# Kernel tuning notes

Hardware: AMD Instinct MI355X
Metric: run time of the kernel (lower is better)

Reference implementation:

```python
import jax, jax.numpy as jnp
import numpy as np
import math

B, S, D, H = 1, 512, 2048, 16
HD = D // H
E, I, G, TKG, TK = 64, 512, 8, 4, 6
SH_I = 2 * I  # n_shared_experts * moe_inter_dim
ROUTE_SCALE = 2.5
EPS = 1e-5
THETA = 500000.0


def rms_norm(x, w):
    return x * jax.lax.rsqrt(jnp.mean(x * x, axis=-1, keepdims=True) + EPS) * w


def rope(x, cos, sin):
    # x: [B,S,H,HD]; complex pairing matches torch.view_as_complex on reshape(..., HD//2, 2)
    xr = x.reshape(x.shape[:-1] + (HD // 2, 2))
    re, im = xr[..., 0], xr[..., 1]
    c = cos[None, :, None, :]
    s = sin[None, :, None, :]
    out = jnp.stack([re * c - im * s, re * s + im * c], axis=-1)
    return out.reshape(x.shape)


def forward(x, freqs_cos, freqs_sin, mask, attn_norm_w, ffn_norm_w,
            wq, wk, wv, wo, gate_w, exp_w1, exp_w2, exp_w3,
            sh_w1, sh_w2, sh_w3):
    # ---- attention sub-block ----
    h = rms_norm(x, attn_norm_w)
    q = (h @ wq.T).reshape(B, S, H, HD)
    k = (h @ wk.T).reshape(B, S, H, HD)
    v = (h @ wv.T).reshape(B, S, H, HD)
    q = rope(q, freqs_cos, freqs_sin)
    k = rope(k, freqs_cos, freqs_sin)
    scores = jnp.einsum('bqhd,bkhd->bhqk', q, k) / math.sqrt(HD) + mask
    p = jax.nn.softmax(scores.astype(jnp.float32), axis=-1).astype(q.dtype)
    attn = jnp.einsum('bhqk,bkhd->bqhd', p, v).reshape(B, S, D)
    x1 = x + attn @ wo.T

    # ---- MoE sub-block ----
    t = rms_norm(x1, ffn_norm_w).reshape(-1, D)  # [T,D]
    T = t.shape[0]
    s = jax.nn.sigmoid(t @ gate_w.T)             # [T,E] sigmoid scoring, bias=None
    sg = s.reshape(T, G, E // G)
    group_scores = sg.max(axis=-1)               # amax per group (bias is None)
    _, gidx = jax.lax.top_k(group_scores, TKG)   # top-4 groups
    keep = jax.nn.one_hot(gidx, G, dtype=s.dtype).sum(axis=1) > 0  # [T,G]
    masked = jnp.where(keep[:, :, None], sg, -jnp.inf).reshape(T, E)
    _, idx = jax.lax.top_k(masked, TK)           # top-6 experts within kept groups
    w = jnp.take_along_axis(s, idx, axis=1)      # gather original scores
    w = w / w.sum(axis=-1, keepdims=True) * ROUTE_SCALE

    # dense combine weights (scatter of top-k routing weights)
    gate_dense = jnp.zeros((T, E), x.dtype).at[jnp.arange(T)[:, None], idx].add(w)

    # routed experts: SwiGLU per expert, weighted combine
    h1 = jnp.einsum('td,eid->tei', t, exp_w1)    # [T,E,I]
    h3 = jnp.einsum('td,eid->tei', t, exp_w3)
    a = jax.nn.silu(h1) * h3
    routed = jnp.einsum('tei,edi,te->td', a, exp_w2, gate_dense)

    # shared experts MLP
    shared = (jax.nn.silu(t @ sh_w1.T) * (t @ sh_w3.T)) @ sh_w2.T

    return x1 + (routed + shared).reshape(B, S, D)


def setup_inputs() -> dict:
    key = jax.random.key(0)
    ks = jax.random.split(key, 12)
    sc = 0.02
    x = jax.random.normal(ks[0], (B, S, D), jnp.float32)
    inv = 1.0 / (THETA ** (jnp.arange(0, HD, 2, dtype=jnp.float32) / HD))
    ang = jnp.arange(S, dtype=jnp.float32)[:, None] * inv[None, :]
    freqs_cos = jnp.cos(ang)
    freqs_sin = jnp.sin(ang)
    mask = jnp.triu(jnp.full((S, S), -1e9, jnp.float32), k=1)[None, None]
    return {
        'x': x,
        'freqs_cos': freqs_cos,
        'freqs_sin': freqs_sin,
        'mask': mask,
        'attn_norm_w': jnp.ones((D,), jnp.float32),
        'ffn_norm_w': jnp.ones((D,), jnp.float32),
        'wq': jax.random.normal(ks[1], (D, D), jnp.float32) * sc,
        'wk': jax.random.normal(ks[2], (D, D), jnp.float32) * sc,
        'wv': jax.random.normal(ks[3], (D, D), jnp.float32) * sc,
        'wo': jax.random.normal(ks[4], (D, D), jnp.float32) * sc,
        'gate_w': jax.random.normal(ks[5], (E, D), jnp.float32) * sc,
        'exp_w1': jax.random.normal(ks[6], (E, I, D), jnp.float32) * sc,
        'exp_w2': jax.random.normal(ks[7], (E, D, I), jnp.float32) * sc,
        'exp_w3': jax.random.normal(ks[8], (E, I, D), jnp.float32) * sc,
        'sh_w1': jax.random.normal(ks[9], (SH_I, D), jnp.float32) * sc,
        'sh_w2': jax.random.normal(ks[10], (D, SH_I), jnp.float32) * sc,
        'sh_w3': jax.random.normal(ks[11], (SH_I, D), jnp.float32) * sc,
    }


def reference(x, freqs_cos, freqs_sin, mask, attn_norm_w, ffn_norm_w,
              wq, wk, wv, wo, gate_w, exp_w1, exp_w2, exp_w3,
              sh_w1, sh_w2, sh_w3):
    return forward(x, freqs_cos, freqs_sin, mask, attn_norm_w, ffn_norm_w,
                   wq, wk, wv, wo, gate_w, exp_w1, exp_w2, exp_w3,
                   sh_w1, sh_w2, sh_w3)
```

## Files before the change

### kernel.cpp

```cpp
#include <hip/hip_runtime.h>
#include <hip/hip_bf16.h>
#include <math.h>

constexpr int S   = 512;
constexpr int D   = 2048;
constexpr int H   = 16;
constexpr int HD  = 128;
constexpr int T   = 512;
constexpr int E   = 64;
constexpr int I_  = 512;
constexpr int G   = 8;
constexpr int TKG = 4;
constexpr int TK  = 6;
constexpr int SH_I = 1024;
constexpr float ROUTE_SCALE = 2.5f;
constexpr float EPS = 1e-5f;

typedef short   s16x8   __attribute__((ext_vector_type(8)));
typedef unsigned short ushort8 __attribute__((ext_vector_type(8)));
typedef float   f32x4   __attribute__((ext_vector_type(4)));

__device__ inline void split8(const float4& x0, const float4& x1, ushort8& h, ushort8& l) {
    float xs[8] = {x0.x, x0.y, x0.z, x0.w, x1.x, x1.y, x1.z, x1.w};
#pragma unroll
    for (int j = 0; j < 8; ++j) {
        __bf16 hb = (__bf16)xs[j];
        float hf = (float)hb;
        __bf16 lb = (__bf16)(xs[j] - hf);
        h[j] = __builtin_bit_cast(unsigned short, hb);
        l[j] = __builtin_bit_cast(unsigned short, lb);
    }
}

__device__ inline s16x8 ldsfrag(const unsigned short* p) {
    return *(const s16x8*)p;
}

__global__ __launch_bounds__(256) void rmsnorm_kernel(const float* __restrict__ x,
                                                      const float* __restrict__ w,
                                                      float* __restrict__ out) {
    int t = blockIdx.x;
    int tid = threadIdx.x;
    const float* row = x + (size_t)t * D;
    float ss = 0.f;
    for (int i = tid; i < D; i += 256) { float v = row[i]; ss += v * v; }
    for (int o = 32; o; o >>= 1) ss += __shfl_down(ss, o, 64);
    __shared__ float red[4];
    if ((tid & 63) == 0) red[tid >> 6] = ss;
    __syncthreads();
    float tot = red[0] + red[1] + red[2] + red[3];
    float scale = rsqrtf(tot / (float)D + EPS);
    for (int i = tid; i < D; i += 256) out[(size_t)t * D + i] = row[i] * scale * w[i];
}

__global__ __launch_bounds__(256) void mgemm_nt_kernel(const float* __restrict__ A,
                                                       const float* __restrict__ B0,
                                                       const float* __restrict__ B1,
                                                       const float* __restrict__ B2,
                                                       float* __restrict__ C0,
                                                       float* __restrict__ C1,
                                                       float* __restrict__ C2,
                                                       const float* __restrict__ addsrc,
                                                       int M, int N, int K) {
    (void)M;
    const float* B = (blockIdx.z == 0) ? B0 : ((blockIdx.z == 1) ? B1 : B2);
    float*       C = (blockIdx.z == 0) ? C0 : ((blockIdx.z == 1) ? C1 : C2);
    __shared__ unsigned short Ah[64][40], Al[64][40], Bh[64][40], Bl[64][40];
    const int m0 = blockIdx.y * 64, n0 = blockIdx.x * 64;
    const int tid = threadIdx.x;
    const int w = tid >> 6, lane = tid & 63;
    const int srow = tid >> 2;
    const int skq  = (tid & 3) * 8;
    const int wm = (w >> 1) * 32, wn = (w & 1) * 32;
    const int fr = lane >> 4, fc = lane & 15;
    const float* Arow = A + (size_t)(m0 + srow) * K + skq;
    const float* Brow = B + (size_t)(n0 + srow) * K + skq;

    f32x4 acc[2][2] = {};
    const int KT = K >> 5;
    float4 pa0 = *(const float4*)(Arow);
    float4 pa1 = *(const float4*)(Arow + 4);
    float4 pb0 = *(const float4*)(Brow);
    float4 pb1 = *(const float4*)(Brow + 4);

    for (int kt = 0; kt < KT; ++kt) {
        __syncthreads();
        {
            ushort8 h, l;
            split8(pa0, pa1, h, l);
            *(ushort8*)&Ah[srow][skq] = h; *(ushort8*)&Al[srow][skq] = l;
            split8(pb0, pb1, h, l);
            *(ushort8*)&Bh[srow][skq] = h; *(ushort8*)&Bl[srow][skq] = l;
        }
        __syncthreads();
        if (kt + 1 < KT) {
            const float* An = Arow + (kt + 1) * 32;
            const float* Bn = Brow + (kt + 1) * 32;
            pa0 = *(const float4*)(An); pa1 = *(const float4*)(An + 4);
            pb0 = *(const float4*)(Bn); pb1 = *(const float4*)(Bn + 4);
        }
        s16x8 fah[2], fal[2], fbh[2], fbl[2];
#pragma unroll
        for (int mf = 0; mf < 2; ++mf) {
            int r = wm + mf * 16 + fc;
            fah[mf] = ldsfrag(&Ah[r][fr * 8]);
            fal[mf] = ldsfrag(&Al[r][fr * 8]);
        }
#pragma unroll
        for (int nf = 0; nf < 2; ++nf) {
            int r = wn + nf * 16 + fc;
            fbh[nf] = ldsfrag(&Bh[r][fr * 8]);
            fbl[nf] = ldsfrag(&Bl[r][fr * 8]);
        }
#pragma unroll
        for (int mf = 0; mf < 2; ++mf)
#pragma unroll
            for (int nf = 0; nf < 2; ++nf) {
                acc[mf][nf] = __builtin_amdgcn_mfma_f32_16x16x32_bf16(fah[mf], fbh[nf], acc[mf][nf], 0, 0, 0);
                acc[mf][nf] = __builtin_amdgcn_mfma_f32_16x16x32_bf16(fah[mf], fbl[nf], acc[mf][nf], 0, 0, 0);
                acc[mf][nf] = __builtin_amdgcn_mfma_f32_16x16x32_bf16(fal[mf], fbh[nf], acc[mf][nf], 0, 0, 0);
            }
    }

#pragma unroll
    for (int mf = 0; mf < 2; ++mf)
#pragma unroll
        for (int nf = 0; nf < 2; ++nf)
#pragma unroll
            for (int r = 0; r < 4; ++r) {
                int gm = m0 + wm + mf * 16 + fr * 4 + r;
                int gn = n0 + wn + nf * 16 + fc;
                size_t off = (size_t)gm * N + gn;
                float v = acc[mf][nf][r];
                if (addsrc) v += addsrc[off];
                C[off] = v;
            }
}

__global__ __launch_bounds__(256) void rope_kernel(float* __restrict__ q, float* __restrict__ k,
                                                   const float* __restrict__ fc,
                                                   const float* __restrict__ fs) {
    int idx = blockIdx.x * 256 + threadIdx.x;
    int p  = idx & (HD / 2 - 1);
    int hh = (idx >> 6) & (H - 1);
    int t  = idx >> 10;
    float c = fc[t * (HD / 2) + p], s = fs[t * (HD / 2) + p];
    size_t base = (size_t)t * D + hh * HD + p * 2;
    float re = q[base], im = q[base + 1];
    q[base]     = re * c - im * s;
    q[base + 1] = re * s + im * c;
    re = k[base]; im = k[base + 1];
    k[base]     = re * c - im * s;
    k[base + 1] = re * s + im * c;
}

__global__ __launch_bounds__(256) void attn_kernel(const float* __restrict__ q,
                                                   const float* __restrict__ k,
                                                   const float* __restrict__ v,
                                                   float* __restrict__ o) {
    int qi = blockIdx.x, hh = blockIdx.y, tid = threadIdx.x;
    __shared__ float qs[HD];
    __shared__ float sc[S];
    __shared__ float redm[4];
    __shared__ float redz[4];
    __shared__ float part[256];
    if (tid < HD) qs[tid] = q[(size_t)qi * D + hh * HD + tid];
    __syncthreads();
    int kn = qi + 1;
    float lmax = -1e30f;
    for (int kk = tid; kk < kn; kk += 256) {
        const float4* k4 = (const float4*)(k + (size_t)kk * D + hh * HD);
        const float4* q4 = (const float4*)qs;
        float s = 0.f;
#pragma unroll
        for (int d4 = 0; d4 < HD / 4; d4++) {
            float4 kvv = k4[d4], qvv = q4[d4];
            s += qvv.x * kvv.x + qvv.y * kvv.y + qvv.z * kvv.z + qvv.w * kvv.w;
        }
        s *= 0.08838834764831845f;
        sc[kk] = s;
        lmax = fmaxf(lmax, s);
    }
    for (int o2 = 32; o2; o2 >>= 1) lmax = fmaxf(lmax, __shfl_down(lmax, o2, 64));
    if ((tid & 63) == 0) redm[tid >> 6] = lmax;
    __syncthreads();
    float M_ = fmaxf(fmaxf(redm[0], redm[1]), fmaxf(redm[2], redm[3]));
    float lsum = 0.f;
    for (int kk = tid; kk < kn; kk += 256) {
        float e2 = expf(sc[kk] - M_);
        sc[kk] = e2;
        lsum += e2;
    }
    for (int o2 = 32; o2; o2 >>= 1) lsum += __shfl_down(lsum, o2, 64);
    if ((tid & 63) == 0) redz[tid >> 6] = lsum;
    __syncthreads();
    float Z = redz[0] + redz[1] + redz[2] + redz[3];
    int d2 = tid & (HD - 1);
    int halfsel = tid >> 7;
    float acc = 0.f;
    for (int kk = halfsel; kk < kn; kk += 2)
        acc += sc[kk] * v[(size_t)kk * D + hh * HD + d2];
    part[tid] = acc;
    __syncthreads();
    if (tid < HD) o[(size_t)qi * D + hh * HD + tid] = (part[tid] + part[tid + HD]) / Z;
}

__global__ __launch_bounds__(256) void gate_kernel(const float* __restrict__ tbuf,
                                                   const float* __restrict__ gate_w,
                                                   float* __restrict__ logits) {
    int tok = blockIdx.x;
    int e    = threadIdx.x >> 2;
    int part = threadIdx.x & 3;
    const float* trow = tbuf   + (size_t)tok * D;
    const float* wrow = gate_w + (size_t)e * D;
    float s = 0.f;
    for (int k = part * 4; k < D; k += 16) {
        float4 a = *(const float4*)(trow + k);
        float4 b = *(const float4*)(wrow + k);
        s += a.x * b.x + a.y * b.y + a.z * b.z + a.w * b.w;
    }
    s += __shfl_down(s, 1, 4);
    s += __shfl_down(s, 2, 4);
    if (part == 0) logits[(size_t)tok * E + e] = s;
}

__global__ __launch_bounds__(64) void routing_kernel(const float* __restrict__ logits,
                                                     float* __restrict__ gw,
                                                     int* __restrict__ counts,
                                                     int* __restrict__ elist) {
    int t = blockIdx.x;
    int lane = threadIdx.x;
    __shared__ float ss[E];
    if (lane < E) ss[lane] = 1.f / (1.f + expf(-logits[(size_t)t * E + lane]));
    __syncthreads();
    if (lane == 0) {
        float gs[G];
        for (int g = 0; g < G; g++) {
            float m = ss[g * 8];
            for (int j = 1; j < 8; j++) m = fmaxf(m, ss[g * 8 + j]);
            gs[g] = m;
        }
        bool keep[G];
        for (int g = 0; g < G; g++) keep[g] = false;
        for (int r = 0; r < TKG; r++) {
            int best = -1; float bv = -1e30f;
            for (int g = 0; g < G; g++)
                if (!keep[g] && gs[g] > bv) { bv = gs[g]; best = g; }
            keep[best] = true;
        }
        float masked[E];
        for (int e2 = 0; e2 < E; e2++) masked[e2] = keep[e2 >> 3] ? ss[e2] : -1e30f;
        int chosen[TK]; float w[TK]; float wsum = 0.f;
        for (int r = 0; r < TK; r++) {
            int best = 0; float bv = -1e31f;
            for (int e2 = 0; e2 < E; e2++)
                if (masked[e2] > bv) { bv = masked[e2]; best = e2; }
            chosen[r] = best; w[r] = ss[best]; masked[best] = -1e31f; wsum += w[r];
        }
        float scale_ = ROUTE_SCALE / wsum;
        for (int r = 0; r < TK; r++) {
            int slot = t * TK + r;
            gw[slot] = w[r] * scale_;
            int e2 = chosen[r];
            int pos = atomicAdd(&counts[e2], 1);
            elist[e2 * T + pos] = slot;
        }
    }
}

__global__ __launch_bounds__(256) void moe_up_kernel(const float* __restrict__ tbuf,
                                                     const float* __restrict__ w1,
                                                     const float* __restrict__ w3,
                                                     const int* __restrict__ counts,
                                                     const int* __restrict__ elist,
                                                     float* __restrict__ abuf) {
    const int e = blockIdx.x;
    const int nt = counts[e];
    if (nt == 0) return;
    const int i0 = blockIdx.y * 64;
    const float* W1 = w1 + (size_t)e * I_ * D;
    const float* W3 = w3 + (size_t)e * I_ * D;
    __shared__ unsigned short Ah[64][40], Al[64][40];
    __shared__ unsigned short B1h[64][40], B1l[64][40];
    __shared__ unsigned short B3h[64][40], B3l[64][40];
    __shared__ int slots[64];
    __shared__ const float* rows[64];
    const int tid = threadIdx.x;
    const int w = tid >> 6, lane = tid & 63;
    const int srow = tid >> 2;
    const int skq  = (tid & 3) * 8;
    const int wm = (w >> 1) * 32, wn = (w & 1) * 32;
    const int fr = lane >> 4, fc = lane & 15;
    const float* B1row = W1 + (size_t)(i0 + srow) * D + skq;
    const float* B3row = W3 + (size_t)(i0 + srow) * D + skq;
    const float4 z4 = make_float4(0.f, 0.f, 0.f, 0.f);
    const int KT = D >> 5;

    for (int tb = 0; tb < nt; tb += 64) {
        if (tid < 64) {
            int sl = (tb + tid < nt) ? elist[e * T + tb + tid] : -1;
            slots[tid] = sl;
            rows[tid] = (sl >= 0) ? (tbuf + (size_t)(sl / TK) * D) : nullptr;
        }
        __syncthreads();
        const float* Ap = rows[srow];
        f32x4 c1[2][2] = {}, c3[2][2] = {};
        float4 pa0, pa1, p10, p11, p30, p31;
        pa0 = Ap ? *(const float4*)(Ap + skq)     : z4;
        pa1 = Ap ? *(const float4*)(Ap + skq + 4) : z4;
        p10 = *(const float4*)(B1row);
        p11 = *(const float4*)(B1row + 4);
        p30 = *(const float4*)(B3row);
        p31 = *(const float4*)(B3row + 4);

        for (int kt = 0; kt < KT; ++kt) {
            __syncthreads();
            {
                ushort8 h, l;
                split8(pa0, pa1, h, l);
                *(ushort8*)&Ah[srow][skq] = h; *(ushort8*)&Al[srow][skq] = l;
                split8(p10, p11, h, l);
                *(ushort8*)&B1h[srow][skq] = h; *(ushort8*)&B1l[srow][skq] = l;
                split8(p30, p31, h, l);
                *(ushort8*)&B3h[srow][skq] = h; *(ushort8*)&B3l[srow][skq] = l;
            }
            __syncthreads();
            if (kt + 1 < KT) {
                const int ko = (kt + 1) * 32 + skq;
                pa0 = Ap ? *(const float4*)(Ap + ko)     : z4;
                pa1 = Ap ? *(const float4*)(Ap + ko + 4) : z4;
                p10 = *(const float4*)(B1row + (kt + 1) * 32);
                p11 = *(const float4*)(B1row + (kt + 1) * 32 + 4);
                p30 = *(const float4*)(B3row + (kt + 1) * 32);
                p31 = *(const float4*)(B3row + (kt + 1) * 32 + 4);
            }
            s16x8 fah[2], fal[2], f1h[2], f1l[2], f3h[2], f3l[2];
#pragma unroll
            for (int mf = 0; mf < 2; ++mf) {
                int r = wm + mf * 16 + fc;
                fah[mf] = ldsfrag(&Ah[r][fr * 8]);
                fal[mf] = ldsfrag(&Al[r][fr * 8]);
            }
#pragma unroll
            for (int nf = 0; nf < 2; ++nf) {
                int r = wn + nf * 16 + fc;
                f1h[nf] = ldsfrag(&B1h[r][fr * 8]);
                f1l[nf] = ldsfrag(&B1l[r][fr * 8]);
                f3h[nf] = ldsfrag(&B3h[r][fr * 8]);
                f3l[nf] = ldsfrag(&B3l[r][fr * 8]);
            }
#pragma unroll
            for (int mf = 0; mf < 2; ++mf)
#pragma unroll
                for (int nf = 0; nf < 2; ++nf) {
                    c1[mf][nf] = __builtin_amdgcn_mfma_f32_16x16x32_bf16(fah[mf], f1h[nf], c1[mf][nf], 0, 0, 0);
                    c1[mf][nf] = __builtin_amdgcn_mfma_f32_16x16x32_bf16(fah[mf], f1l[nf], c1[mf][nf], 0, 0, 0);
                    c1[mf][nf] = __builtin_amdgcn_mfma_f32_16x16x32_bf16(fal[mf], f1h[nf], c1[mf][nf], 0, 0, 0);
                    c3[mf][nf] = __builtin_amdgcn_mfma_f32_16x16x32_bf16(fah[mf], f3h[nf], c3[mf][nf], 0, 0, 0);
                    c3[mf][nf] = __builtin_amdgcn_mfma_f32_16x16x32_bf16(fah[mf], f3l[nf], c3[mf][nf], 0, 0, 0);
                    c3[mf][nf] = __builtin_amdgcn_mfma_f32_16x16x32_bf16(fal[mf], f3h[nf], c3[mf][nf], 0, 0, 0);
                }
        }

#pragma unroll
        for (int mf = 0; mf < 2; ++mf)
#pragma unroll
            for (int nf = 0; nf < 2; ++nf)
#pragma unroll
                for (int r = 0; r < 4; ++r) {
                    int mrow = wm + mf * 16 + fr * 4 + r;
                    if (tb + mrow < nt) {
                        int sl = slots[mrow];
                        float h1 = c1[mf][nf][r];
                        float h3 = c3[mf][nf][r];
                        float o = (h1 / (1.f + expf(-h1))) * h3;
                        abuf[(size_t)sl * I_ + i0 + wn + nf * 16 + fc] = o;
                    }
                }
        __syncthreads();
    }
}

__global__ __launch_bounds__(256) void moe_down_kernel(const float* __restrict__ abuf,
                                                       const float* __restrict__ w2,
                                                       const int* __restrict__ counts,
                                                       const int* __restrict__ elist,
                                                       const float* __restrict__ gw,
                                                       float* __restrict__ routed) {
    const int e = blockIdx.x;
    const int nt = counts[e];
    if (nt == 0) return;
    const int d0 = blockIdx.y * 64;
    const float* W2 = w2 + (size_t)e * D * I_;
    __shared__ unsigned short Ah[64][40], Al[64][40], Bh[64][40], Bl[64][40];
    __shared__ int slots[64];
    __shared__ const float* rows[64];
    const int tid = threadIdx.x;
    const int w = tid >> 6, lane = tid & 63;
    const int srow = tid >> 2;
    const int skq  = (tid & 3) * 8;
    const int wm = (w >> 1) * 32, wn = (w & 1) * 32;
    const int fr = lane >> 4, fc = lane & 15;
    const float* Brow = W2 + (size_t)(d0 + srow) * I_ + skq;
    const float4 z4 = make_float4(0.f, 0.f, 0.f, 0.f);
    const int KT = I_ >> 5;

    for (int tb = 0; tb < nt; tb += 64) {
        if (tid < 64) {
            int sl = (tb + tid < nt) ? elist[e * T + tb + tid] : -1;
            slots[tid] = sl;
            rows[tid] = (sl >= 0) ? (abuf + (size_t)sl * I_) : nullptr;
        }
        __syncthreads();
        const float* Ap = rows[srow];
        f32x4 acc[2][2] = {};
        float4 pa0, pa1, pb0, pb1;
        pa0 = Ap ? *(const float4*)(Ap + skq)     : z4;
        pa1 = Ap ? *(const float4*)(Ap + skq + 4) : z4;
        pb0 = *(const float4*)(Brow);
        pb1 = *(const float4*)(Brow + 4);

        for (int kt = 0; kt < KT; ++kt) {
            __syncthreads();
            {
                ushort8 h, l;
                split8(pa0, pa1, h, l);
                *(ushort8*)&Ah[srow][skq] = h; *(ushort8*)&Al[srow][skq] = l;
                split8(pb0, pb1, h, l);
                *(ushort8*)&Bh[srow][skq] = h; *(ushort8*)&Bl[srow][skq] = l;
            }
            __syncthreads();
            if (kt + 1 < KT) {
                const int ko = (kt + 1) * 32 + skq;
                pa0 = Ap ? *(const float4*)(Ap + ko)     : z4;
                pa1 = Ap ? *(const float4*)(Ap + ko + 4) : z4;
                pb0 = *(const float4*)(Brow + (kt + 1) * 32);
                pb1 = *(const float4*)(Brow + (kt + 1) * 32 + 4);
            }
            s16x8 fah[2], fal[2], fbh[2], fbl[2];
#pragma unroll
            for (int mf = 0; mf < 2; ++mf) {
                int r = wm + mf * 16 + fc;
                fah[mf] = ldsfrag(&Ah[r][fr * 8]);
                fal[mf] = ldsfrag(&Al[r][fr * 8]);
            }
#pragma unroll
            for (int nf = 0; nf < 2; ++nf) {
                int r = wn + nf * 16 + fc;
                fbh[nf] = ldsfrag(&Bh[r][fr * 8]);
                fbl[nf] = ldsfrag(&Bl[r][fr * 8]);
            }
#pragma unroll
            for (int mf = 0; mf < 2; ++mf)
#pragma unroll
                for (int nf = 0; nf < 2; ++nf) {
                    acc[mf][nf] = __builtin_amdgcn_mfma_f32_16x16x32_bf16(fah[mf], fbh[nf], acc[mf][nf], 0, 0, 0);
                    acc[mf][nf] = __builtin_amdgcn_mfma_f32_16x16x32_bf16(fah[mf], fbl[nf], acc[mf][nf], 0, 0, 0);
                    acc[mf][nf] = __builtin_amdgcn_mfma_f32_16x16x32_bf16(fal[mf], fbh[nf], acc[mf][nf], 0, 0, 0);
                }
        }

#pragma unroll
        for (int mf = 0; mf < 2; ++mf)
#pragma unroll
            for (int nf = 0; nf < 2; ++nf)
#pragma unroll
                for (int r = 0; r < 4; ++r) {
                    int mrow = wm + mf * 16 + fr * 4 + r;
                    if (tb + mrow < nt) {
                        int sl = slots[mrow];
                        float g = gw[sl];
                        int t = sl / TK;
                        atomicAdd(&routed[(size_t)t * D + d0 + wn + nf * 16 + fc], g * acc[mf][nf][r]);
                    }
                }
        __syncthreads();
    }
}

__global__ __launch_bounds__(256) void silu_mul_kernel(const float* __restrict__ a,
                                                       const float* __restrict__ b,
                                                       float* __restrict__ o, int n) {
    int i = blockIdx.x * 256 + threadIdx.x;
    if (i < n) { float x = a[i]; o[i] = x / (1.f + expf(-x)) * b[i]; }
}

__global__ __launch_bounds__(256) void add_inplace_kernel(float* __restrict__ o,
                                                          const float* __restrict__ a, int n) {
    int i = blockIdx.x * 256 + threadIdx.x;
    if (i < n) o[i] += a[i];
}

extern "C" void kernel_launch(void* const* d_in, const int* in_sizes, int n_in,
                              void* d_out, int out_size, void* d_ws, size_t ws_size,
                              hipStream_t stream) {
    (void)in_sizes; (void)n_in; (void)out_size; (void)ws_size;
    const float* x      = (const float*)d_in[0];
    const float* fc     = (const float*)d_in[1];
    const float* fs     = (const float*)d_in[2];
    const float* anw    = (const float*)d_in[4];
    const float* fnw    = (const float*)d_in[5];
    const float* wq     = (const float*)d_in[6];
    const float* wk     = (const float*)d_in[7];
    const float* wv     = (const float*)d_in[8];
    const float* wo     = (const float*)d_in[9];
    const float* gate_w = (const float*)d_in[10];
    const float* ew1    = (const float*)d_in[11];
    const float* ew2    = (const float*)d_in[12];
    const float* ew3    = (const float*)d_in[13];
    const float* sw1    = (const float*)d_in[14];
    const float* sw2    = (const float*)d_in[15];
    const float* sw3    = (const float*)d_in[16];
    float* out = (float*)d_out;

    char* wsp = (char*)d_ws;
    size_t off = 0;
    auto alloc = [&](size_t bytes) {
        void* p = wsp + off;
        off += (bytes + 255) & ~(size_t)255;
        return p;
    };
    float* hbuf   = (float*)alloc((size_t)T * D * 4);
    float* qbuf   = (float*)alloc((size_t)T * D * 4);
    float* kbuf   = (float*)alloc((size_t)T * D * 4);
    float* vbuf   = (float*)alloc((size_t)T * D * 4);
    float* attnb  = (float*)alloc((size_t)T * D * 4);
    float* x1     = (float*)alloc((size_t)T * D * 4);
    float* tbuf   = (float*)alloc((size_t)T * D * 4);
    float* routed = (float*)alloc((size_t)T * D * 4);
    float* logits = (float*)alloc((size_t)T * E * 4);
    float* gwbuf  = (float*)alloc((size_t)T * TK * 4);
    int*   counts = (int*)alloc(E * 4);
    int*   elist  = (int*)alloc((size_t)E * T * 4);
    float* abuf   = (float*)alloc((size_t)T * TK * I_ * 4);
    float* u1     = (float*)alloc((size_t)T * SH_I * 4);
    float* u3     = (float*)alloc((size_t)T * SH_I * 4);
    float* ub     = (float*)alloc((size_t)T * SH_I * 4);

    hipMemsetAsync(counts, 0, E * 4, stream);
    hipMemsetAsync(routed, 0, (size_t)T * D * 4, stream);

    rmsnorm_kernel<<<T, 256, 0, stream>>>(x, anw, hbuf);
    mgemm_nt_kernel<<<dim3(D / 64, T / 64, 3), 256, 0, stream>>>(hbuf, wq, wk, wv,
                                                                 qbuf, kbuf, vbuf,
                                                                 nullptr, T, D, D);
    rope_kernel<<<(T * H * HD / 2) / 256, 256, 0, stream>>>(qbuf, kbuf, fc, fs);
    attn_kernel<<<dim3(S, H), 256, 0, stream>>>(qbuf, kbuf, vbuf, attnb);
    mgemm_nt_kernel<<<dim3(D / 64, T / 64, 1), 256, 0, stream>>>(attnb, wo, wo, wo,
                                                                 x1, x1, x1,
                                                                 x, T, D, D);

    rmsnorm_kernel<<<T, 256, 0, stream>>>(x1, fnw, tbuf);
    gate_kernel<<<T, 256, 0, stream>>>(tbuf, gate_w, logits);
    routing_kernel<<<T, 64, 0, stream>>>(logits, gwbuf, counts, elist);
    moe_up_kernel<<<dim3(E, I_ / 64), 256, 0, stream>>>(tbuf, ew1, ew3, counts, elist, abuf);
    moe_down_kernel<<<dim3(E, D / 64), 256, 0, stream>>>(abuf, ew2, counts, elist, gwbuf, routed);

    mgemm_nt_kernel<<<dim3(SH_I / 64, T / 64, 2), 256, 0, stream>>>(tbuf, sw1, sw3, sw3,
                                                                    u1, u3, u3,
                                                                    nullptr, T, SH_I, D);
    silu_mul_kernel<<<(T * SH_I) / 256, 256, 0, stream>>>(u1, u3, ub, T * SH_I);
    mgemm_nt_kernel<<<dim3(D / 64, T / 64, 1), 256, 0, stream>>>(ub, sw2, sw2, sw2,
                                                                 out, out, out,
                                                                 x1, T, D, SH_I);
    add_inplace_kernel<<<(T * D) / 256, 256, 0, stream>>>(out, routed, T * D);
}
```

Before: 1.678 ms.

## Replace scalar attention with tiled flash-attention using split-bf16 MFMA

```diff
diff --git a/kernel.cpp b/kernel.cpp
--- a/kernel.cpp
+++ b/kernel.cpp
@@ -34,6 +34,10 @@
 
 __device__ inline s16x8 ldsfrag(const unsigned short* p) {
     return *(const s16x8*)p;
+}
+
+__device__ inline s16x8 as_s16(ushort8 u) {
+    return __builtin_bit_cast(s16x8, u);
 }
 
 __global__ __launch_bounds__(256) void rmsnorm_kernel(const float* __restrict__ x,
@@ -154,55 +158,133 @@
     k[base + 1] = re * s + im * c;
 }
 
-__global__ __launch_bounds__(256) void attn_kernel(const float* __restrict__ q,
-                                                   const float* __restrict__ k,
-                                                   const float* __restrict__ v,
-                                                   float* __restrict__ o) {
-    int qi = blockIdx.x, hh = blockIdx.y, tid = threadIdx.x;
-    __shared__ float qs[HD];
-    __shared__ float sc[S];
-    __shared__ float redm[4];
-    __shared__ float redz[4];
-    __shared__ float part[256];
-    if (tid < HD) qs[tid] = q[(size_t)qi * D + hh * HD + tid];
-    __syncthreads();
-    int kn = qi + 1;
-    float lmax = -1e30f;
-    for (int kk = tid; kk < kn; kk += 256) {
-        const float4* k4 = (const float4*)(k + (size_t)kk * D + hh * HD);
-        const float4* q4 = (const float4*)qs;
-        float s = 0.f;
-#pragma unroll
-        for (int d4 = 0; d4 < HD / 4; d4++) {
-            float4 kvv = k4[d4], qvv = q4[d4];
-            s += qvv.x * kvv.x + qvv.y * kvv.y + qvv.z * kvv.z + qvv.w * kvv.w;
-        }
-        s *= 0.08838834764831845f;
-        sc[kk] = s;
-        lmax = fmaxf(lmax, s);
-    }
-    for (int o2 = 32; o2; o2 >>= 1) lmax = fmaxf(lmax, __shfl_down(lmax, o2, 64));
-    if ((tid & 63) == 0) redm[tid >> 6] = lmax;
-    __syncthreads();
-    float M_ = fmaxf(fmaxf(redm[0], redm[1]), fmaxf(redm[2], redm[3]));
-    float lsum = 0.f;
-    for (int kk = tid; kk < kn; kk += 256) {
-        float e2 = expf(sc[kk] - M_);
-        sc[kk] = e2;
-        lsum += e2;
-    }
-    for (int o2 = 32; o2; o2 >>= 1) lsum += __shfl_down(lsum, o2, 64);
-    if ((tid & 63) == 0) redz[tid >> 6] = lsum;
-    __syncthreads();
-    float Z = redz[0] + redz[1] + redz[2] + redz[3];
-    int d2 = tid & (HD - 1);
-    int halfsel = tid >> 7;
-    float acc = 0.f;
-    for (int kk = halfsel; kk < kn; kk += 2)
-        acc += sc[kk] * v[(size_t)kk * D + hh * HD + d2];
-    part[tid] = acc;
-    __syncthreads();
-    if (tid < HD) o[(size_t)qi * D + hh * HD + tid] = (part[tid] + part[tid + HD]) / Z;
+__global__ __launch_bounds__(256) void attn_mfma_kernel(const float* __restrict__ q,
+                                                        const float* __restrict__ k,
+                                                        const float* __restrict__ v,
+                                                        float* __restrict__ o) {
+    const int qt = blockIdx.x, h = blockIdx.y;
+    const int q0 = qt * 64;
+    const int tid = threadIdx.x;
+    const int w = tid >> 6, lane = tid & 63;
+    const int fc = lane & 15, fr = lane >> 4;
+    __shared__ unsigned short Kh[4][32][40], Kl[4][32][40];
+    __shared__ unsigned short Vth[128][44], Vtl[128][44];
+    __shared__ unsigned short Pbh[4][16][38], Pbl[4][16][38];
+
+    ushort8 qh[4], ql[4];
+    {
+        const float* qrow = q + (size_t)(q0 + w * 16 + fc) * D + h * HD;
+#pragma unroll
+        for (int ks = 0; ks < 4; ++ks) {
+            float4 a = *(const float4*)(qrow + ks * 32 + fr * 8);
+            float4 b = *(const float4*)(qrow + ks * 32 + fr * 8 + 4);
+            split8(a, b, qh[ks], ql[ks]);
+        }
+    }
+
+    f32x4 accO[8] = {};
+    float mold[4] = {-3e38f, -3e38f, -3e38f, -3e38f};
+    float lsum[4] = {};
+    const int NT = 2 * qt + 2;
+
+    for (int kt = 0; kt < NT; ++kt) {
+        const int k0 = kt * 32;
+        __syncthreads();
+#pragma unroll
+        for (int rep = 0; rep < 2; ++rep) {
+            int e = rep * 256 + tid;
+            int key = e >> 4;
+            int dq  = (e & 15) * 8;
+            const float* kr = k + (size_t)(k0 + key) * D + h * HD + dq;
+            const float* vr = v + (size_t)(k0 + key) * D + h * HD + dq;
+            float4 a = *(const float4*)kr, b = *(const float4*)(kr + 4);
+            ushort8 hh, ll;
+            split8(a, b, hh, ll);
+            *(ushort8*)&Kh[dq >> 5][key][dq & 31] = hh;
+            *(ushort8*)&Kl[dq >> 5][key][dq & 31] = ll;
+            a = *(const float4*)vr; b = *(const float4*)(vr + 4);
+            split8(a, b, hh, ll);
+#pragma unroll
+            for (int j = 0; j < 8; ++j) { Vth[dq + j][key] = hh[j]; Vtl[dq + j][key] = ll[j]; }
+        }
+        __syncthreads();
+
+        f32x4 sc[2] = {};
+#pragma unroll
+        for (int kf = 0; kf < 2; ++kf) {
+#pragma unroll
+            for (int ks = 0; ks < 4; ++ks) {
+                s16x8 kbh = ldsfrag(&Kh[ks][kf * 16 + fc][fr * 8]);
+                s16x8 kbl = ldsfrag(&Kl[ks][kf * 16 + fc][fr * 8]);
+                sc[kf] = __builtin_amdgcn_mfma_f32_16x16x32_bf16(as_s16(qh[ks]), kbh, sc[kf], 0, 0, 0);
+                sc[kf] = __builtin_amdgcn_mfma_f32_16x16x32_bf16(as_s16(qh[ks]), kbl, sc[kf], 0, 0, 0);
+                sc[kf] = __builtin_amdgcn_mfma_f32_16x16x32_bf16(as_s16(ql[ks]), kbh, sc[kf], 0, 0, 0);
+            }
+        }
+
+        const bool diag = (k0 + 31 > q0);
+        float p2[2][4], fscv[4];
+#pragma unroll
+        for (int r = 0; r < 4; ++r) {
+            const int qrow = q0 + w * 16 + fr * 4 + r;
+#pragma unroll
+            for (int kf = 0; kf < 2; ++kf) {
+                float sv = sc[kf][r] * 0.08838834764831845f;
+                if (diag && (k0 + kf * 16 + fc) > qrow) sv = -3e38f;
+                sc[kf][r] = sv;
+            }
+            float mx = fmaxf(sc[0][r], sc[1][r]);
+            mx = fmaxf(mx, __shfl_xor(mx, 1, 64));
+            mx = fmaxf(mx, __shfl_xor(mx, 2, 64));
+            mx = fmaxf(mx, __shfl_xor(mx, 4, 64));
+            mx = fmaxf(mx, __shfl_xor(mx, 8, 64));
+            float mn = fmaxf(mold[r], mx);
+            float fs = expf(mold[r] - mn);
+            float s0 = expf(sc[0][r] - mn);
+            float s1 = expf(sc[1][r] - mn);
+            p2[0][r] = s0; p2[1][r] = s1;
+            float rs = s0 + s1;
+            rs += __shfl_xor(rs, 1, 64);
+            rs += __shfl_xor(rs, 2, 64);
+            rs += __shfl_xor(rs, 4, 64);
+            rs += __shfl_xor(rs, 8, 64);
+            lsum[r] = lsum[r] * fs + rs;
+            mold[r] = mn; fscv[r] = fs;
+        }
+#pragma unroll
+        for (int df = 0; df < 8; ++df)
+#pragma unroll
+            for (int r = 0; r < 4; ++r) accO[df][r] *= fscv[r];
+
+#pragma unroll
+        for (int kf = 0; kf < 2; ++kf)
+#pragma unroll
+            for (int r = 0; r < 4; ++r) {
+                __bf16 hb = (__bf16)p2[kf][r];
+                float hf = (float)hb;
+                __bf16 lb = (__bf16)(p2[kf][r] - hf);
+                Pbh[w][fr * 4 + r][kf * 16 + fc] = __builtin_bit_cast(unsigned short, hb);
+                Pbl[w][fr * 4 + r][kf * 16 + fc] = __builtin_bit_cast(unsigned short, lb);
+            }
+        s16x8 pah = ldsfrag(&Pbh[w][fc][fr * 8]);
+        s16x8 pal = ldsfrag(&Pbl[w][fc][fr * 8]);
+#pragma unroll
+        for (int df = 0; df < 8; ++df) {
+            s16x8 vbh = ldsfrag(&Vth[df * 16 + fc][fr * 8]);
+            s16x8 vbl = ldsfrag(&Vtl[df * 16 + fc][fr * 8]);
+            accO[df] = __builtin_amdgcn_mfma_f32_16x16x32_bf16(pah, vbh, accO[df], 0, 0, 0);
+            accO[df] = __builtin_amdgcn_mfma_f32_16x16x32_bf16(pah, vbl, accO[df], 0, 0, 0);
+            accO[df] = __builtin_amdgcn_mfma_f32_16x16x32_bf16(pal, vbh, accO[df], 0, 0, 0);
+        }
+    }
+
+#pragma unroll
+    for (int df = 0; df < 8; ++df)
+#pragma unroll
+        for (int r = 0; r < 4; ++r) {
+            int qrow = q0 + w * 16 + fr * 4 + r;
+            o[(size_t)qrow * D + h * HD + df * 16 + fc] = accO[df][r] / lsum[r];
+        }
 }
 
 __global__ __launch_bounds__(256) void gate_kernel(const float* __restrict__ tbuf,
@@ -545,7 +627,7 @@
                                                                  qbuf, kbuf, vbuf,
                                                                  nullptr, T, D, D);
     rope_kernel<<<(T * H * HD / 2) / 256, 256, 0, stream>>>(qbuf, kbuf, fc, fs);
-    attn_kernel<<<dim3(S, H), 256, 0, stream>>>(qbuf, kbuf, vbuf, attnb);
+    attn_mfma_kernel<<<dim3(S / 64, H), 256, 0, stream>>>(qbuf, kbuf, vbuf, attnb);
     mgemm_nt_kernel<<<dim3(D / 64, T / 64, 1), 256, 0, stream>>>(attnb, wo, wo, wo,
                                                                  x1, x1, x1,
                                                                  x, T, D, D);
```

Result: faster. 1.398 ms (-16.7%).
